# Optimization experiments

Measured on AMD Instinct MI355X. Metric: run time of the kernel, lower is better.

Reference implementation:

```python
import jax, jax.numpy as jnp
import numpy as np

# Mistral-7B layer-0 config
D, DKV, DFF, NH, NKV, HD, BLK, VOCAB = 4096, 1024, 14336, 32, 8, 128, 64, 32000
THETA = 10000.0
NF4_CODE = jnp.array([-1.0, -0.6961928009986877, -0.5250730514526367, -0.39491748809814453,
                      -0.28444138169288635, -0.18477343022823334, -0.09105003625154495, 0.0,
                      0.07958029955625534, 0.16093020141124725, 0.24611230194568634,
                      0.33791524171829224, 0.44070982933044434, 0.5626170039176941,
                      0.7229568362236023, 1.0], dtype=jnp.float32)


def dequant_nf4(idx, absmax):
    # idx: int [out,in] 4-bit codes; absmax: [numel/BLK] blockwise scales
    w = jnp.take(NF4_CODE, idx.reshape(-1, BLK)) * absmax[:, None]
    return w.reshape(idx.shape)


def rmsnorm(x, w, eps=1e-5):
    return x * jax.lax.rsqrt(jnp.mean(x * x, axis=-1, keepdims=True) + eps) * w


def rope(x, pos):
    # x: [B,S,H,HD] -- HF rotate-half convention
    half = HD // 2
    inv = 1.0 / (THETA ** (jnp.arange(0, half, dtype=jnp.float32) / half))
    f = pos[:, None] * inv[None, :]                      # [S, half]
    cos = jnp.concatenate([jnp.cos(f), jnp.cos(f)], -1)[None, :, None, :]
    sin = jnp.concatenate([jnp.sin(f), jnp.sin(f)], -1)[None, :, None, :]
    x1, x2 = x[..., :half], x[..., half:]
    rot = jnp.concatenate([-x2, x1], -1)
    return x * cos + rot * sin


def setup_inputs() -> dict:
    key = jax.random.key(0)
    ks = jax.random.split(key, 20)
    B, S = 4, 512
    inp = {}
    inp["input_ids"] = jax.random.randint(ks[0], (B, S), 0, VOCAB, dtype=jnp.int32)
    inp["attention_mask"] = jnp.ones((B, S), dtype=jnp.int32)
    inp["embed_table"] = jax.random.normal(ks[1], (VOCAB, D), dtype=jnp.float32) * 0.02
    shapes = {"q": (D, D), "k": (DKV, D), "v": (DKV, D), "o": (D, D),
              "gate": (DFF, D), "up": (DFF, D), "down": (D, DFF)}
    for i, (n, sh) in enumerate(shapes.items()):
        inp["idx_" + n] = jax.random.randint(ks[2 + i], sh, 0, 16, dtype=jnp.int32)
        inp["absmax_" + n] = jax.random.uniform(ks[9 + i], (sh[0] * sh[1] // BLK,), dtype=jnp.float32) * 0.02
    inp["rms1_w"] = jnp.ones((D,), jnp.float32)
    inp["rms2_w"] = jnp.ones((D,), jnp.float32)
    inp["dp_w"] = jax.random.normal(ks[16], (50, D), jnp.float32) * 0.02
    inp["dp_b"] = jnp.zeros((50,), jnp.float32)
    return inp


def reference(input_ids, attention_mask, embed_table,
              idx_q, idx_k, idx_v, idx_o, idx_gate, idx_up, idx_down,
              absmax_q, absmax_k, absmax_v, absmax_o, absmax_gate, absmax_up, absmax_down,
              rms1_w, rms2_w, dp_w, dp_b):
    B, S = input_ids.shape
    h = embed_table[input_ids]                            # [B,S,D]

    # --- Mistral decoder layer 0 (hidden_states[1]) ---
    r = rmsnorm(h, rms1_w)
    Wq = dequant_nf4(idx_q, absmax_q)
    Wk = dequant_nf4(idx_k, absmax_k)
    Wv = dequant_nf4(idx_v, absmax_v)
    Wo = dequant_nf4(idx_o, absmax_o)
    q = (r @ Wq.T).reshape(B, S, NH, HD)
    k = (r @ Wk.T).reshape(B, S, NKV, HD)
    v = (r @ Wv.T).reshape(B, S, NKV, HD)
    pos = jnp.arange(S, dtype=jnp.float32)
    q, k = rope(q, pos), rope(k, pos)
    rep = NH // NKV
    k = jnp.repeat(k, rep, axis=2)
    v = jnp.repeat(v, rep, axis=2)
    scores = jnp.einsum('bqhd,bkhd->bhqk', q, k) / np.float32(np.sqrt(HD))
    causal = jnp.tril(jnp.ones((S, S), bool))
    m = causal[None, None] & (attention_mask[:, None, None, :] > 0)
    scores = jnp.where(m, scores, jnp.float32(-1e9))
    p = jax.nn.softmax(scores, axis=-1)
    ao = jnp.einsum('bhqk,bkhd->bqhd', p, v).reshape(B, S, D)
    h = h + ao @ Wo.T

    r2 = rmsnorm(h, rms2_w)
    Wg = dequant_nf4(idx_gate, absmax_gate)
    Wu = dequant_nf4(idx_up, absmax_up)
    Wd = dequant_nf4(idx_down, absmax_down)
    h = h + (jax.nn.silu(r2 @ Wg.T) * (r2 @ Wu.T)) @ Wd.T

    # --- last_token_pool + L2 normalize ---
    last = jnp.sum(attention_mask, axis=-1) - 1           # [B]
    pooled = h[jnp.arange(B), last]                       # [B,D]
    pooled = pooled / jnp.maximum(jnp.linalg.norm(pooled, axis=1, keepdims=True), 1e-12)

    # --- down_projection + query*entity node embeddings ---
    emb = pooled @ dp_w.T + dp_b                          # [B,50]
    bs = B // 2
    node = emb[:bs] * emb[bs:]                            # [bs,50]
    return node
```

## Files before the change

kernel.cpp:

```cpp
#include <hip/hip_runtime.h>
#include <stdint.h>
#include <math.h>

#define TOK 2048
#define DMODEL 4096
#define DFF 14336
#define SEQ 512

typedef float f32x4 __attribute__((ext_vector_type(4)));
typedef short s16x8 __attribute__((ext_vector_type(8)));
typedef unsigned short u16x8 __attribute__((ext_vector_type(8)));

__constant__ float NF4_TAB[16] = {
  -1.0f, -0.6961928009986877f, -0.5250730514526367f, -0.39491748809814453f,
  -0.28444138169288635f, -0.18477343022823334f, -0.09105003625154495f, 0.0f,
  0.07958029955625534f, 0.16093020141124725f, 0.24611230194568634f,
  0.33791524171829224f, 0.44070982933044434f, 0.5626170039176941f,
  0.7229568362236023f, 1.0f };

__device__ __forceinline__ uint16_t f2bf(float f) {
  union { float f; uint32_t u; } x; x.f = f;
  uint32_t r = (x.u + 0x7FFFu + ((x.u >> 16) & 1u)) >> 16;
  return (uint16_t)r;
}
__device__ __forceinline__ float bf2f(uint16_t u) {
  union { uint32_t u; float f; } x; x.u = ((uint32_t)u) << 16;
  return x.f;
}
__device__ __forceinline__ f32x4 mfma16(s16x8 a, s16x8 b, f32x4 c) {
  return __builtin_amdgcn_mfma_f32_16x16x32_bf16(a, b, c, 0, 0, 0);
}
__device__ __forceinline__ void gload_lds16(const void* g, void* l) {
  __builtin_amdgcn_global_load_lds(
    (const __attribute__((address_space(1))) unsigned int*)g,
    (__attribute__((address_space(3))) unsigned int*)l, 16, 0, 0);
}

__global__ __launch_bounds__(256) void k_last(const int* __restrict__ maskp,
                                              int* __restrict__ lastb)
{
  int wv = threadIdx.x >> 6, l = threadIdx.x & 63;
  int cnt = 0;
  for (int j = l; j < SEQ; j += 64) cnt += (maskp[wv * SEQ + j] > 0);
  #pragma unroll
  for (int off = 1; off < 64; off <<= 1) cnt += __shfl_xor(cnt, off);
  if (l == 0) lastb[wv] = cnt - 1;
}

__global__ __launch_bounds__(256) void k_dequant(const int* __restrict__ idx,
    const float* __restrict__ am, uint16_t* __restrict__ out, int nelems, int K)
{
  __shared__ float code[16];
  if (threadIdx.x < 16) code[threadIdx.x] = NF4_TAB[threadIdx.x];
  __syncthreads();
  int nch = nelems >> 3;
  int stride = gridDim.x * 256;
  for (int c = blockIdx.x * 256 + threadIdx.x; c < nch; c += stride) {
    int e = c << 3;
    int row = e / K;
    int kc = e - row * K;
    float a = am[c >> 3];
    int4 i0 = *(const int4*)(idx + e);
    int4 i1 = *(const int4*)(idx + e + 4);
    u16x8 pk;
    pk[0] = f2bf(code[i0.x] * a);
    pk[1] = f2bf(code[i0.y] * a);
    pk[2] = f2bf(code[i0.z] * a);
    pk[3] = f2bf(code[i0.w] * a);
    pk[4] = f2bf(code[i1.x] * a);
    pk[5] = f2bf(code[i1.y] * a);
    pk[6] = f2bf(code[i1.z] * a);
    pk[7] = f2bf(code[i1.w] * a);
    int dk = (kc & ~63) | (((((kc >> 3) & 7) ^ (row & 7))) << 3);
    *(u16x8*)(out + (size_t)row * K + dk) = pk;
  }
}

__global__ __launch_bounds__(256) void k_rms(const int* __restrict__ ids,
    const float* __restrict__ table, const float* __restrict__ w,
    uint16_t* __restrict__ r)
{
  int t = blockIdx.x, tid = threadIdx.x;
  int wv = tid >> 6, l = tid & 63;
  const float* src = table + (size_t)ids[t] * DMODEL;
  int d0 = tid * 16;
  float vals[16];
  float ss = 0.f;
  #pragma unroll
  for (int i = 0; i < 4; ++i) {
    float4 v4 = *(const float4*)(src + d0 + i * 4);
    vals[i*4+0] = v4.x; vals[i*4+1] = v4.y; vals[i*4+2] = v4.z; vals[i*4+3] = v4.w;
    ss += v4.x*v4.x + v4.y*v4.y + v4.z*v4.z + v4.w*v4.w;
  }
  #pragma unroll
  for (int off = 1; off < 64; off <<= 1) ss += __shfl_xor(ss, off);
  __shared__ float red[4];
  if (l == 0) red[wv] = ss;
  __syncthreads();
  float rs = rsqrtf((red[0]+red[1]+red[2]+red[3]) * (1.f/DMODEL) + 1e-5f);
  #pragma unroll
  for (int cth = 0; cth < 2; ++cth) {
    int dd = d0 + cth * 8;
    u16x8 pk;
    #pragma unroll
    for (int j = 0; j < 8; ++j) pk[j] = f2bf(vals[cth*8+j] * rs * w[dd + j]);
    int dsw = (dd & ~63) | (((((dd >> 3) & 7) ^ (t & 7))) << 3);
    *(u16x8*)(r + (size_t)t * DMODEL + dsw) = pk;
  }
}

__global__ __launch_bounds__(512, 2) void k_gemmkv(
    const uint16_t* __restrict__ A, const uint16_t* __restrict__ W,
    float* __restrict__ pout)
{
  constexpr int K = 4096;
  constexpr int NT = 16;
  __shared__ __align__(1024) uint16_t As_[2 * 256 * 64];
  __shared__ __align__(1024) uint16_t Bs_[2 * 256 * 64];
  const int tid = threadIdx.x;
  const int wid = tid >> 6, l = tid & 63;
  const int wr = wid >> 2, wc = wid & 3;
  const int n0 = blockIdx.x * 256, m0 = blockIdx.y * 256;
  const size_t kbase = blockIdx.z * 1024;
  const int lrow = l >> 3, lcb = (l & 7) * 16;

  auto stA = [&](int t, int h) {
    int ta = (t < NT) ? t : (t - NT);
    const char* g = (const char*)A +
        ((size_t)(m0 + h * 128 + wid * 16 + lrow) * K + kbase + ta * 64) * 2 + lcb;
    char* s = (char*)As_ + (t & 1) * 32768 + h * 16384 + wid * 2048;
    gload_lds16(g, s);
    gload_lds16(g + (size_t)8 * K * 2, s + 1024);
  };
  auto stB = [&](int t, int h) {
    int ta = (t < NT) ? t : (t - NT);
    const char* g = (const char*)W +
        ((size_t)(n0 + h * 128 + wid * 16 + lrow) * K + kbase + ta * 64) * 2 + lcb;
    char* s = (char*)Bs_ + (t & 1) * 32768 + h * 16384 + wid * 2048;
    gload_lds16(g, s);
    gload_lds16(g + (size_t)8 * K * 2, s + 1024);
  };

  const int cb0 = (((l >> 4) << 4)) ^ ((l & 7) << 4);
  const int cb1 = (64 + ((l >> 4) << 4)) ^ ((l & 7) << 4);

  const f32x4 Z4 = {0.f, 0.f, 0.f, 0.f};
  f32x4 acc[8][4];
  #pragma unroll
  for (int i = 0; i < 8; ++i)
    #pragma unroll
    for (int j = 0; j < 4; ++j) acc[i][j] = Z4;
  s16x8 bfr[4][2];

#define VMW asm volatile("s_waitcnt vmcnt(6)" ::: "memory")
#define PHASE(DB, Q, READB, STG) {                                          \
    const char* abase = (const char*)As_ + (DB) * 32768;                    \
    s16x8 af[2][2];                                                         \
    _Pragma("unroll") for (int mm = 0; mm < 2; ++mm) {                      \
      int arow = ((2 * (2 * (Q) + mm) + wr) * 16 + (l & 15)) * 128;         \
      af[mm][0] = *(const s16x8*)(abase + arow + cb0);                      \
      af[mm][1] = *(const s16x8*)(abase + arow + cb1);                      \
    }                                                                       \
    if (READB) {                                                            \
      const char* bbase = (const char*)Bs_ + (DB) * 32768;                  \
      _Pragma("unroll") for (int nn = 0; nn < 4; ++nn) {                    \
        int brow = (wc * 64 + nn * 16 + (l & 15)) * 128;                    \
        bfr[nn][0] = *(const s16x8*)(bbase + brow + cb0);                   \
        bfr[nn][1] = *(const s16x8*)(bbase + brow + cb1);                   \
      }                                                                     \
    }                                                                       \
    STG;                                                                    \
    __builtin_amdgcn_s_barrier();                                           \
    asm volatile("s_waitcnt lgkmcnt(0)" ::: "memory");                      \
    __builtin_amdgcn_sched_barrier(0);                                      \
    __builtin_amdgcn_s_setprio(1);                                          \
    _Pragma("unroll") for (int mm = 0; mm < 2; ++mm)                        \
      _Pragma("unroll") for (int nn = 0; nn < 4; ++nn) {                    \
        acc[2 * (Q) + mm][nn] = mfma16(af[mm][0], bfr[nn][0], acc[2 * (Q) + mm][nn]); \
        acc[2 * (Q) + mm][nn] = mfma16(af[mm][1], bfr[nn][1], acc[2 * (Q) + mm][nn]); \
      }                                                                     \
    __builtin_amdgcn_s_setprio(0);                                          \
    __builtin_amdgcn_s_barrier();                                           \
  }

  stB(0, 0); stA(0, 0); stB(0, 1); stA(0, 1);
  stB(1, 0); stA(1, 0); stB(1, 1);
  VMW;
  __builtin_amdgcn_s_barrier();

  for (int it = 0; it < NT / 2; ++it) {
    int t0 = 2 * it, t1 = t0 + 1;
    PHASE(0, 0, 1, stA(t1, 1));
    PHASE(0, 1, 0, stB(t0 + 2, 0));
    PHASE(0, 2, 0, stA(t0 + 2, 0));
    PHASE(0, 3, 0, { stB(t0 + 2, 1); VMW; });
    PHASE(1, 0, 1, stA(t0 + 2, 1));
    PHASE(1, 1, 0, stB(t1 + 2, 0));
    PHASE(1, 2, 0, stA(t1 + 2, 0));
    PHASE(1, 3, 0, { stB(t1 + 2, 1); VMW; });
  }
  asm volatile("s_waitcnt vmcnt(0)" ::: "memory");
  __builtin_amdgcn_s_barrier();
#undef PHASE
#undef VMW

  float* po = pout + (size_t)blockIdx.z * 2048 * 2048;
  #pragma unroll
  for (int mf = 0; mf < 8; ++mf)
    #pragma unroll
    for (int nf = 0; nf < 4; ++nf)
      #pragma unroll
      for (int r = 0; r < 4; ++r) {
        int row = m0 + (2 * mf + wr) * 16 + ((l >> 4) << 2) + r;
        int col = n0 + wc * 64 + nf * 16 + (l & 15);
        po[(size_t)row * 2048 + col] = acc[mf][nf][r];
      }
}

__global__ __launch_bounds__(256) void k_redrope(const float* __restrict__ p,
    uint16_t* __restrict__ kv)
{
  int t = blockIdx.x, tid = threadIdx.x;
  const size_t zs = (size_t)2048 * 2048;
  auto sum4 = [&](int c) -> float {
    size_t o = (size_t)t * 2048 + c;
    return p[o] + p[o + zs] + p[o + 2 * zs] + p[o + 3 * zs];
  };
  float pos = (float)(t & (SEQ - 1));
  for (int pi = tid; pi < 512; pi += 256) {
    int hh = pi >> 6, j = pi & 63;
    int c1 = hh * 128 + j, c2 = c1 + 64;
    float s1 = sum4(c1), s2 = sum4(c2);
    float f = pos * expf(-(float)j * 0.14391156831212787f);
    float sn, cs;
    sincosf(f, &sn, &cs);
    kv[(size_t)t * 2048 + c1] = f2bf(s1 * cs - s2 * sn);
    kv[(size_t)t * 2048 + c2] = f2bf(s2 * cs + s1 * sn);
  }
  for (int c = 1024 + tid; c < 2048; c += 256)
    kv[(size_t)t * 2048 + c] = f2bf(sum4(c));
}

__global__ __launch_bounds__(256) void k_prep_r4(const uint16_t* __restrict__ rbuf,
    const int* __restrict__ lastb, float* __restrict__ r4i)
{
  int r = blockIdx.x;
  int t = r * SEQ + lastb[r];
  const uint16_t* src = rbuf + (size_t)t * DMODEL;
  for (int k = threadIdx.x * 8; k < DMODEL; k += 2048) {
    int so = (k & ~63) | (((((k >> 3) & 7) ^ (t & 7))) << 3);
    u16x8 v = *(const u16x8*)(src + so);
    #pragma unroll
    for (int j = 0; j < 8; ++j) r4i[(k + j) * 4 + r] = bf2f(v[j]);
  }
}

template<int MODE>
__global__ __launch_bounds__(256) void k_gemv4i(const int* __restrict__ idx,
    const float* __restrict__ am, const float* __restrict__ a4i,
    float* __restrict__ out4i, const float* __restrict__ table,
    const int* __restrict__ ids, const int* __restrict__ lastb)
{
  __shared__ float code[16];
  if (threadIdx.x < 16) code[threadIdx.x] = NF4_TAB[threadIdx.x];
  __syncthreads();
  int wv = threadIdx.x >> 6, l = threadIdx.x & 63;
  int lhi = l >> 4;
  int n = blockIdx.x * 4 + wv;
  const int4* ip = (const int4*)(idx + (size_t)n * 4096);
  const float* ap = am + (size_t)n * 64;
  float a0 = 0.f, a1 = 0.f, a2 = 0.f, a3 = 0.f;
  #pragma unroll
  for (int kk = 0; kk < 16; ++kk) {
    int4 iv = ip[kk * 64 + l];
    float sc = ap[kk * 4 + lhi];
    float w0 = code[iv.x] * sc, w1 = code[iv.y] * sc;
    float w2 = code[iv.z] * sc, w3 = code[iv.w] * sc;
    const float* A0 = a4i + (kk * 256 + l * 4) * 4;
    f32x4 k0 = *(const f32x4*)(A0);
    f32x4 k1 = *(const f32x4*)(A0 + 4);
    f32x4 k2 = *(const f32x4*)(A0 + 8);
    f32x4 k3 = *(const f32x4*)(A0 + 12);
    a0 = fmaf(w0, k0[0], fmaf(w1, k1[0], fmaf(w2, k2[0], fmaf(w3, k3[0], a0))));
    a1 = fmaf(w0, k0[1], fmaf(w1, k1[1], fmaf(w2, k2[1], fmaf(w3, k3[1], a1))));
    a2 = fmaf(w0, k0[2], fmaf(w1, k1[2], fmaf(w2, k2[2], fmaf(w3, k3[2], a2))));
    a3 = fmaf(w0, k0[3], fmaf(w1, k1[3], fmaf(w2, k2[3], fmaf(w3, k3[3], a3))));
  }
  #pragma unroll
  for (int off = 1; off < 64; off <<= 1) {
    a0 += __shfl_xor(a0, off); a1 += __shfl_xor(a1, off);
    a2 += __shfl_xor(a2, off); a3 += __shfl_xor(a3, off);
  }
  if (l == 0) {
    f32x4 o;
    o[0] = a0; o[1] = a1; o[2] = a2; o[3] = a3;
    if (MODE == 1) {
      #pragma unroll
      for (int r = 0; r < 4; ++r)
        o[r] += table[(size_t)ids[r * SEQ + lastb[r]] * DMODEL + n];
    }
    *(f32x4*)(out4i + (size_t)n * 4) = o;
  }
}

__global__ __launch_bounds__(256) void k_gemv_gu(const int* __restrict__ idxg,
    const float* __restrict__ amg, const int* __restrict__ idxu,
    const float* __restrict__ amu, const float* __restrict__ a4i,
    float* __restrict__ hm4i)
{
  __shared__ float code[16];
  if (threadIdx.x < 16) code[threadIdx.x] = NF4_TAB[threadIdx.x];
  __syncthreads();
  int wv = threadIdx.x >> 6, l = threadIdx.x & 63;
  int lhi = l >> 4;
  int n = blockIdx.x * 4 + wv;
  const int4* ipg = (const int4*)(idxg + (size_t)n * 4096);
  const int4* ipu = (const int4*)(idxu + (size_t)n * 4096);
  const float* apg = amg + (size_t)n * 64;
  const float* apu = amu + (size_t)n * 64;
  float g0 = 0.f, g1 = 0.f, g2 = 0.f, g3 = 0.f;
  float u0 = 0.f, u1 = 0.f, u2 = 0.f, u3 = 0.f;
  #pragma unroll
  for (int kk = 0; kk < 16; ++kk) {
    int4 ig = ipg[kk * 64 + l];
    int4 iu = ipu[kk * 64 + l];
    float sg = apg[kk * 4 + lhi];
    float su = apu[kk * 4 + lhi];
    float wg0 = code[ig.x] * sg, wg1 = code[ig.y] * sg;
    float wg2 = code[ig.z] * sg, wg3 = code[ig.w] * sg;
    float wu0 = code[iu.x] * su, wu1 = code[iu.y] * su;
    float wu2 = code[iu.z] * su, wu3 = code[iu.w] * su;
    const float* A0 = a4i + (kk * 256 + l * 4) * 4;
    f32x4 k0 = *(const f32x4*)(A0);
    f32x4 k1 = *(const f32x4*)(A0 + 4);
    f32x4 k2 = *(const f32x4*)(A0 + 8);
    f32x4 k3 = *(const f32x4*)(A0 + 12);
    g0 = fmaf(wg0, k0[0], fmaf(wg1, k1[0], fmaf(wg2, k2[0], fmaf(wg3, k3[0], g0))));
    g1 = fmaf(wg0, k0[1], fmaf(wg1, k1[1], fmaf(wg2, k2[1], fmaf(wg3, k3[1], g1))));
    g2 = fmaf(wg0, k0[2], fmaf(wg1, k1[2], fmaf(wg2, k2[2], fmaf(wg3, k3[2], g2))));
    g3 = fmaf(wg0, k0[3], fmaf(wg1, k1[3], fmaf(wg2, k2[3], fmaf(wg3, k3[3], g3))));
    u0 = fmaf(wu0, k0[0], fmaf(wu1, k1[0], fmaf(wu2, k2[0], fmaf(wu3, k3[0], u0))));
    u1 = fmaf(wu0, k0[1], fmaf(wu1, k1[1], fmaf(wu2, k2[1], fmaf(wu3, k3[1], u1))));
    u2 = fmaf(wu0, k0[2], fmaf(wu1, k1[2], fmaf(wu2, k2[2], fmaf(wu3, k3[2], u2))));
    u3 = fmaf(wu0, k0[3], fmaf(wu1, k1[3], fmaf(wu2, k2[3], fmaf(wu3, k3[3], u3))));
  }
  #pragma unroll
  for (int off = 1; off < 64; off <<= 1) {
    g0 += __shfl_xor(g0, off); g1 += __shfl_xor(g1, off);
    g2 += __shfl_xor(g2, off); g3 += __shfl_xor(g3, off);
    u0 += __shfl_xor(u0, off); u1 += __shfl_xor(u1, off);
    u2 += __shfl_xor(u2, off); u3 += __shfl_xor(u3, off);
  }
  if (l == 0) {
    f32x4 o;
    o[0] = (g0 / (1.f + __expf(-g0))) * u0;
    o[1] = (g1 / (1.f + __expf(-g1))) * u1;
    o[2] = (g2 / (1.f + __expf(-g2))) * u2;
    o[3] = (g3 / (1.f + __expf(-g3))) * u3;
    *(f32x4*)(hm4i + (size_t)n * 4) = o;
  }
}

__global__ __launch_bounds__(256) void k_gemv_down(const int* __restrict__ idx,
    const float* __restrict__ am, const float* __restrict__ hm4i,
    const float* __restrict__ h4i, float* __restrict__ h4r)
{
  __shared__ float code[16];
  if (threadIdx.x < 16) code[threadIdx.x] = NF4_TAB[threadIdx.x];
  __syncthreads();
  int wv = threadIdx.x >> 6, l = threadIdx.x & 63;
  int lhi = l >> 4;
  int n = blockIdx.x * 4 + wv;
  const int4* ip = (const int4*)(idx + (size_t)n * 14336);
  const float* ap = am + (size_t)n * 224;
  float a0 = 0.f, a1 = 0.f, a2 = 0.f, a3 = 0.f;
  #pragma unroll 8
  for (int kk = 0; kk < 56; ++kk) {
    int4 iv = ip[kk * 64 + l];
    float sc = ap[kk * 4 + lhi];
    float w0 = code[iv.x] * sc, w1 = code[iv.y] * sc;
    float w2 = code[iv.z] * sc, w3 = code[iv.w] * sc;
    const float* A0 = hm4i + (kk * 256 + l * 4) * 4;
    f32x4 k0 = *(const f32x4*)(A0);
    f32x4 k1 = *(const f32x4*)(A0 + 4);
    f32x4 k2 = *(const f32x4*)(A0 + 8);
    f32x4 k3 = *(const f32x4*)(A0 + 12);
    a0 = fmaf(w0, k0[0], fmaf(w1, k1[0], fmaf(w2, k2[0], fmaf(w3, k3[0], a0))));
    a1 = fmaf(w0, k0[1], fmaf(w1, k1[1], fmaf(w2, k2[1], fmaf(w3, k3[1], a1))));
    a2 = fmaf(w0, k0[2], fmaf(w1, k1[2], fmaf(w2, k2[2], fmaf(w3, k3[2], a2))));
    a3 = fmaf(w0, k0[3], fmaf(w1, k1[3], fmaf(w2, k2[3], fmaf(w3, k3[3], a3))));
  }
  #pragma unroll
  for (int off = 1; off < 64; off <<= 1) {
    a0 += __shfl_xor(a0, off); a1 += __shfl_xor(a1, off);
    a2 += __shfl_xor(a2, off); a3 += __shfl_xor(a3, off);
  }
  if (l == 0) {
    f32x4 hr = *(const f32x4*)(h4i + (size_t)n * 4);
    h4r[0 * 4096 + n] = hr[0] + a0;
    h4r[1 * 4096 + n] = hr[1] + a1;
    h4r[2 * 4096 + n] = hr[2] + a2;
    h4r[3 * 4096 + n] = hr[3] + a3;
  }
}

__global__ __launch_bounds__(256) void k_attn4(const float* __restrict__ q4i,
    const uint16_t* __restrict__ kv, const int* __restrict__ maskp,
    const int* __restrict__ lastb, float* __restrict__ ao4i)
{
  int hh = blockIdx.x, b = blockIdx.y;
  int kvh = hh >> 2;
  int tid = threadIdx.x;
  __shared__ float qs[128];
  __shared__ float sarr[512];
  __shared__ float red[256];
  __shared__ float oacc[2][128];
  int last = lastb[b];
  if (tid < 128) {
    int d = tid, j = d & 63;
    float f = (float)last * expf(-(float)j * 0.14391156831212787f);
    float sn, cs;
    sincosf(f, &sn, &cs);
    float qd  = q4i[(hh * 128 + d) * 4 + b];
    float qd2 = (d < 64) ? q4i[(hh * 128 + d + 64) * 4 + b]
                         : q4i[(hh * 128 + d - 64) * 4 + b];
    float v = (d < 64) ? (qd * cs - qd2 * sn) : (qd * cs + qd2 * sn);
    qs[d] = v * 0.08838834764831845f;
  }
  __syncthreads();
  float sl[2];
  #pragma unroll
  for (int h2 = 0; h2 < 2; ++h2) {
    int jj = tid + h2 * 256;
    bool valid = (jj <= last) && (maskp[b * SEQ + jj] > 0);
    float s = -1e9f;
    if (valid) {
      s = 0.f;
      const uint16_t* kp = kv + ((size_t)(b * SEQ + jj)) * 2048 + kvh * 128;
      #pragma unroll
      for (int c = 0; c < 16; ++c) {
        u16x8 kvv = *(const u16x8*)(kp + c * 8);
        #pragma unroll
        for (int e = 0; e < 8; ++e)
          s = fmaf(qs[c * 8 + e], bf2f(kvv[e]), s);
      }
    }
    sarr[jj] = s;
    sl[h2] = s;
  }
  red[tid] = fmaxf(sl[0], sl[1]);
  __syncthreads();
  for (int s = 128; s > 0; s >>= 1) {
    if (tid < s) red[tid] = fmaxf(red[tid], red[tid + s]);
    __syncthreads();
  }
  float m = red[0];
  __syncthreads();
  float ps = 0.f;
  #pragma unroll
  for (int h2 = 0; h2 < 2; ++h2) {
    int jj = tid + h2 * 256;
    float pe = __expf(sarr[jj] - m);
    ps += pe;
    sarr[jj] = pe;
  }
  red[tid] = ps;
  __syncthreads();
  for (int s = 128; s > 0; s >>= 1) {
    if (tid < s) red[tid] += red[tid + s];
    __syncthreads();
  }
  float inv = 1.f / red[0];
  __syncthreads();
  int half = tid >> 7, d = tid & 127;
  float acc = 0.f;
  const uint16_t* vp = kv + ((size_t)(b * SEQ + half * 256)) * 2048 + 1024 + kvh * 128 + d;
  for (int j = 0; j < 256; ++j)
    acc = fmaf(sarr[half * 256 + j], bf2f(vp[(size_t)j * 2048]), acc);
  oacc[half][d] = acc;
  __syncthreads();
  if (tid < 128)
    ao4i[(hh * 128 + tid) * 4 + b] = (oacc[0][tid] + oacc[1][tid]) * inv;
}

__global__ __launch_bounds__(256) void k_rms2i(const float* __restrict__ h4i,
    const float* __restrict__ w, float* __restrict__ r2i)
{
  int tid = threadIdx.x, wv = tid >> 6, l = tid & 63;
  f32x4 vals[16];
  f32x4 ss = {0.f, 0.f, 0.f, 0.f};
  #pragma unroll
  for (int i = 0; i < 16; ++i) {
    vals[i] = *(const f32x4*)(h4i + (size_t)(tid + i * 256) * 4);
    ss += vals[i] * vals[i];
  }
  #pragma unroll
  for (int off = 1; off < 64; off <<= 1) {
    ss[0] += __shfl_xor(ss[0], off);
    ss[1] += __shfl_xor(ss[1], off);
    ss[2] += __shfl_xor(ss[2], off);
    ss[3] += __shfl_xor(ss[3], off);
  }
  __shared__ f32x4 red[4];
  if (l == 0) red[wv] = ss;
  __syncthreads();
  f32x4 tot = red[0] + red[1] + red[2] + red[3];
  f32x4 rs;
  #pragma unroll
  for (int r = 0; r < 4; ++r) rs[r] = rsqrtf(tot[r] * (1.f / 4096.f) + 1e-5f);
  #pragma unroll
  for (int i = 0; i < 16; ++i) {
    float wk = w[tid + i * 256];
    f32x4 o = vals[i] * rs * wk;
    *(f32x4*)(r2i + (size_t)(tid + i * 256) * 4) = o;
  }
}

__global__ __launch_bounds__(256) void k_pool3(const float* __restrict__ h4r,
    const float* __restrict__ dpw, const float* __restrict__ dpb,
    float* __restrict__ out)
{
  int o = blockIdx.x;
  int tid = threadIdx.x, wv = tid >> 6, l = tid & 63;
  __shared__ float dsh[4], nsh[4];
  const float* row = h4r + wv * 4096;
  const float* wrow = dpw + (size_t)o * 4096;
  float d1 = 0.f, ss = 0.f;
  for (int d = l * 4; d < 4096; d += 256) {
    float4 v = *(const float4*)(row + d);
    float4 u = *(const float4*)(wrow + d);
    d1 += v.x*u.x + v.y*u.y + v.z*u.z + v.w*u.w;
    ss += v.x*v.x + v.y*v.y + v.z*v.z + v.w*v.w;
  }
  #pragma unroll
  for (int off = 1; off < 64; off <<= 1) {
    d1 += __shfl_xor(d1, off);
    ss += __shfl_xor(ss, off);
  }
  if (l == 0) { dsh[wv] = d1; nsh[wv] = fmaxf(sqrtf(ss), 1e-12f); }
  __syncthreads();
  if (tid < 2) {
    float b = dpb[o];
    float e1 = dsh[tid] / nsh[tid] + b;
    float e2 = dsh[tid + 2] / nsh[tid + 2] + b;
    out[tid * 50 + o] = e1 * e2;
  }
}

extern "C" void kernel_launch(void* const* d_in, const int* in_sizes, int n_in,
                              void* d_out, int out_size, void* d_ws, size_t ws_size,
                              hipStream_t stream) {
  const int*   ids   = (const int*)d_in[0];
  const int*   maskp = (const int*)d_in[1];
  const float* table = (const float*)d_in[2];
  const int* idxp[7];
  const float* amp[7];
  if (in_sizes[4] == in_sizes[3] / 64) {
    for (int i = 0; i < 7; ++i) {
      idxp[i] = (const int*)d_in[3 + 2 * i];
      amp[i]  = (const float*)d_in[4 + 2 * i];
    }
  } else {
    for (int i = 0; i < 7; ++i) {
      idxp[i] = (const int*)d_in[3 + i];
      amp[i]  = (const float*)d_in[10 + i];
    }
  }
  const float* rms1 = (const float*)d_in[17];
  const float* rms2w = (const float*)d_in[18];
  const float* dpw  = (const float*)d_in[19];
  const float* dpb  = (const float*)d_in[20];
  float* out = (float*)d_out;

  char* p = (char*)d_ws;
  int*      lastb = (int*)p;      p += 256;
  float*    r4i   = (float*)p;    p += 4 * 4096 * 4;
  float*    q4i   = (float*)p;    p += 4 * 4096 * 4;
  float*    ao4i  = (float*)p;    p += 4 * 4096 * 4;
  float*    h4i   = (float*)p;    p += 4 * 4096 * 4;
  float*    r2i   = (float*)p;    p += 4 * 4096 * 4;
  float*    h4r   = (float*)p;    p += 4 * 4096 * 4;
  float*    hm4i  = (float*)p;    p += (size_t)4 * DFF * 4 + 512;
  uint16_t* kvbuf = (uint16_t*)p; p += (size_t)TOK * 2048 * 2;
  uint16_t* rbuf  = (uint16_t*)p; p += (size_t)TOK * DMODEL * 2;
  uint16_t* wbuf  = (uint16_t*)p; p += (size_t)2048 * DMODEL * 2;
  float*    pbuf  = (float*)p;    p += (size_t)4 * 2048 * 2048 * 4;

  k_last<<<1, 256, 0, stream>>>(maskp, lastb);
  k_rms<<<TOK, 256, 0, stream>>>(ids, table, rms1, rbuf);

  k_dequant<<<2048, 256, 0, stream>>>(idxp[1], amp[1], wbuf, 1024 * DMODEL, DMODEL);
  k_dequant<<<2048, 256, 0, stream>>>(idxp[2], amp[2], wbuf + (size_t)1024 * DMODEL, 1024 * DMODEL, DMODEL);
  k_gemmkv<<<dim3(8, 8, 4), 512, 0, stream>>>(rbuf, wbuf, pbuf);
  k_redrope<<<TOK, 256, 0, stream>>>(pbuf, kvbuf);

  k_prep_r4<<<4, 256, 0, stream>>>(rbuf, lastb, r4i);
  k_gemv4i<0><<<1024, 256, 0, stream>>>(idxp[0], amp[0], r4i, q4i, nullptr, nullptr, nullptr);

  k_attn4<<<dim3(32, 4), 256, 0, stream>>>(q4i, kvbuf, maskp, lastb, ao4i);

  k_gemv4i<1><<<1024, 256, 0, stream>>>(idxp[3], amp[3], ao4i, h4i, table, ids, lastb);

  k_rms2i<<<1, 256, 0, stream>>>(h4i, rms2w, r2i);
  k_gemv_gu<<<3584, 256, 0, stream>>>(idxp[4], amp[4], idxp[5], amp[5], r2i, hm4i);
  k_gemv_down<<<1024, 256, 0, stream>>>(idxp[6], amp[6], hm4i, h4i, h4r);

  k_pool3<<<50, 256, 0, stream>>>(h4r, dpw, dpb, out);
}
```

Before: 415.6 us.

## Merge independent kernels into block-range fused launches and use packed f32x2 FMAs

```diff
diff --git a/kernel.cpp b/kernel.cpp
--- a/kernel.cpp
+++ b/kernel.cpp
@@ -8,6 +8,7 @@
 #define SEQ 512
 
 typedef float f32x4 __attribute__((ext_vector_type(4)));
+typedef float f32x2 __attribute__((ext_vector_type(2)));
 typedef short s16x8 __attribute__((ext_vector_type(8)));
 typedef unsigned short u16x8 __attribute__((ext_vector_type(8)));
 
@@ -35,77 +36,85 @@
     (const __attribute__((address_space(1))) unsigned int*)g,
     (__attribute__((address_space(3))) unsigned int*)l, 16, 0, 0);
 }
-
-__global__ __launch_bounds__(256) void k_last(const int* __restrict__ maskp,
-                                              int* __restrict__ lastb)
-{
-  int wv = threadIdx.x >> 6, l = threadIdx.x & 63;
-  int cnt = 0;
-  for (int j = l; j < SEQ; j += 64) cnt += (maskp[wv * SEQ + j] > 0);
-  #pragma unroll
-  for (int off = 1; off < 64; off <<= 1) cnt += __shfl_xor(cnt, off);
-  if (l == 0) lastb[wv] = cnt - 1;
-}
-
-__global__ __launch_bounds__(256) void k_dequant(const int* __restrict__ idx,
-    const float* __restrict__ am, uint16_t* __restrict__ out, int nelems, int K)
-{
-  __shared__ float code[16];
-  if (threadIdx.x < 16) code[threadIdx.x] = NF4_TAB[threadIdx.x];
-  __syncthreads();
-  int nch = nelems >> 3;
-  int stride = gridDim.x * 256;
-  for (int c = blockIdx.x * 256 + threadIdx.x; c < nch; c += stride) {
-    int e = c << 3;
-    int row = e / K;
-    int kc = e - row * K;
-    float a = am[c >> 3];
-    int4 i0 = *(const int4*)(idx + e);
-    int4 i1 = *(const int4*)(idx + e + 4);
-    u16x8 pk;
-    pk[0] = f2bf(code[i0.x] * a);
-    pk[1] = f2bf(code[i0.y] * a);
-    pk[2] = f2bf(code[i0.z] * a);
-    pk[3] = f2bf(code[i0.w] * a);
-    pk[4] = f2bf(code[i1.x] * a);
-    pk[5] = f2bf(code[i1.y] * a);
-    pk[6] = f2bf(code[i1.z] * a);
-    pk[7] = f2bf(code[i1.w] * a);
-    int dk = (kc & ~63) | (((((kc >> 3) & 7) ^ (row & 7))) << 3);
-    *(u16x8*)(out + (size_t)row * K + dk) = pk;
-  }
-}
-
-__global__ __launch_bounds__(256) void k_rms(const int* __restrict__ ids,
-    const float* __restrict__ table, const float* __restrict__ w,
-    uint16_t* __restrict__ r)
-{
-  int t = blockIdx.x, tid = threadIdx.x;
-  int wv = tid >> 6, l = tid & 63;
-  const float* src = table + (size_t)ids[t] * DMODEL;
-  int d0 = tid * 16;
-  float vals[16];
-  float ss = 0.f;
-  #pragma unroll
-  for (int i = 0; i < 4; ++i) {
-    float4 v4 = *(const float4*)(src + d0 + i * 4);
-    vals[i*4+0] = v4.x; vals[i*4+1] = v4.y; vals[i*4+2] = v4.z; vals[i*4+3] = v4.w;
-    ss += v4.x*v4.x + v4.y*v4.y + v4.z*v4.z + v4.w*v4.w;
-  }
-  #pragma unroll
-  for (int off = 1; off < 64; off <<= 1) ss += __shfl_xor(ss, off);
-  __shared__ float red[4];
-  if (l == 0) red[wv] = ss;
-  __syncthreads();
-  float rs = rsqrtf((red[0]+red[1]+red[2]+red[3]) * (1.f/DMODEL) + 1e-5f);
-  #pragma unroll
-  for (int cth = 0; cth < 2; ++cth) {
-    int dd = d0 + cth * 8;
-    u16x8 pk;
-    #pragma unroll
-    for (int j = 0; j < 8; ++j) pk[j] = f2bf(vals[cth*8+j] * rs * w[dd + j]);
-    int dsw = (dd & ~63) | (((((dd >> 3) & 7) ^ (t & 7))) << 3);
-    *(u16x8*)(r + (size_t)t * DMODEL + dsw) = pk;
+__device__ __forceinline__ f32x2 pf(float w, f32x2 v, f32x2 acc) {
+  f32x2 wv = {w, w};
+  return wv * v + acc;
+}
+
+__global__ __launch_bounds__(256) void k_fusedA(const int* __restrict__ ids,
+    const float* __restrict__ table, const float* __restrict__ w1,
+    uint16_t* __restrict__ rbuf, const int* __restrict__ idxK,
+    const float* __restrict__ amK, const int* __restrict__ idxV,
+    const float* __restrict__ amV, uint16_t* __restrict__ wbuf,
+    const int* __restrict__ maskp, int* __restrict__ lastb)
+{
+  int bid = blockIdx.x, tid = threadIdx.x;
+  if (bid < 2048) {
+    int t = bid;
+    int wv = tid >> 6, l = tid & 63;
+    const float* src = table + (size_t)ids[t] * DMODEL;
+    int d0 = tid * 16;
+    float vals[16];
+    float ss = 0.f;
+    #pragma unroll
+    for (int i = 0; i < 4; ++i) {
+      float4 v4 = *(const float4*)(src + d0 + i * 4);
+      vals[i*4+0] = v4.x; vals[i*4+1] = v4.y; vals[i*4+2] = v4.z; vals[i*4+3] = v4.w;
+      ss += v4.x*v4.x + v4.y*v4.y + v4.z*v4.z + v4.w*v4.w;
+    }
+    #pragma unroll
+    for (int off = 1; off < 64; off <<= 1) ss += __shfl_xor(ss, off);
+    __shared__ float red[4];
+    if (l == 0) red[wv] = ss;
+    __syncthreads();
+    float rs = rsqrtf((red[0]+red[1]+red[2]+red[3]) * (1.f/DMODEL) + 1e-5f);
+    #pragma unroll
+    for (int cth = 0; cth < 2; ++cth) {
+      int dd = d0 + cth * 8;
+      u16x8 pk;
+      #pragma unroll
+      for (int j = 0; j < 8; ++j) pk[j] = f2bf(vals[cth*8+j] * rs * w1[dd + j]);
+      int dsw = (dd & ~63) | (((((dd >> 3) & 7) ^ (t & 7))) << 3);
+      *(u16x8*)(rbuf + (size_t)t * DMODEL + dsw) = pk;
+    }
+  } else if (bid < 3072) {
+    bool isV = bid >= 2560;
+    const int* idx = isV ? idxV : idxK;
+    const float* am = isV ? amV : amK;
+    uint16_t* out = wbuf + (isV ? (size_t)1024 * DMODEL : 0);
+    int base = bid - (isV ? 2560 : 2048);
+    __shared__ float code[16];
+    if (tid < 16) code[tid] = NF4_TAB[tid];
+    __syncthreads();
+    const int nch = 1024 * DMODEL / 8;
+    for (int c = base * 256 + tid; c < nch; c += 512 * 256) {
+      int e = c << 3;
+      int row = e >> 12;
+      int kc = e & 4095;
+      float a = am[c >> 3];
+      int4 i0 = *(const int4*)(idx + e);
+      int4 i1 = *(const int4*)(idx + e + 4);
+      u16x8 pk;
+      pk[0] = f2bf(code[i0.x] * a);
+      pk[1] = f2bf(code[i0.y] * a);
+      pk[2] = f2bf(code[i0.z] * a);
+      pk[3] = f2bf(code[i0.w] * a);
+      pk[4] = f2bf(code[i1.x] * a);
+      pk[5] = f2bf(code[i1.y] * a);
+      pk[6] = f2bf(code[i1.z] * a);
+      pk[7] = f2bf(code[i1.w] * a);
+      int dk = (kc & ~63) | (((((kc >> 3) & 7) ^ (row & 7))) << 3);
+      *(u16x8*)(out + (size_t)row * DMODEL + dk) = pk;
+    }
+  } else {
+    int b = bid - 3072;
+    if (tid < 64) {
+      int cnt = 0;
+      for (int j = tid; j < SEQ; j += 64) cnt += (maskp[b * SEQ + j] > 0);
+      #pragma unroll
+      for (int off = 1; off < 64; off <<= 1) cnt += __shfl_xor(cnt, off);
+      if (tid == 0) lastb[b] = cnt - 1;
+    }
   }
 }
 
@@ -120,8 +129,12 @@
   const int tid = threadIdx.x;
   const int wid = tid >> 6, l = tid & 63;
   const int wr = wid >> 2, wc = wid & 3;
-  const int n0 = blockIdx.x * 256, m0 = blockIdx.y * 256;
-  const size_t kbase = blockIdx.z * 1024;
+  int f = blockIdx.x + (blockIdx.y << 3) + (blockIdx.z << 6);
+  int fs = ((f & 7) << 5) + (f >> 3);
+  const int n0 = (fs & 7) * 256;
+  const int m0 = ((fs >> 3) & 7) * 256;
+  const int zq = fs >> 6;
+  const size_t kbase = (size_t)zq * 1024;
   const int lrow = l >> 3, lcb = (l & 7) * 16;
 
   auto stA = [&](int t, int h) {
@@ -204,7 +217,7 @@
 #undef PHASE
 #undef VMW
 
-  float* po = pout + (size_t)blockIdx.z * 2048 * 2048;
+  float* po = pout + (size_t)zq * 2048 * 2048;
   #pragma unroll
   for (int mf = 0; mf < 8; ++mf)
     #pragma unroll
@@ -217,30 +230,6 @@
       }
 }
 
-__global__ __launch_bounds__(256) void k_redrope(const float* __restrict__ p,
-    uint16_t* __restrict__ kv)
-{
-  int t = blockIdx.x, tid = threadIdx.x;
-  const size_t zs = (size_t)2048 * 2048;
-  auto sum4 = [&](int c) -> float {
-    size_t o = (size_t)t * 2048 + c;
-    return p[o] + p[o + zs] + p[o + 2 * zs] + p[o + 3 * zs];
-  };
-  float pos = (float)(t & (SEQ - 1));
-  for (int pi = tid; pi < 512; pi += 256) {
-    int hh = pi >> 6, j = pi & 63;
-    int c1 = hh * 128 + j, c2 = c1 + 64;
-    float s1 = sum4(c1), s2 = sum4(c2);
-    float f = pos * expf(-(float)j * 0.14391156831212787f);
-    float sn, cs;
-    sincosf(f, &sn, &cs);
-    kv[(size_t)t * 2048 + c1] = f2bf(s1 * cs - s2 * sn);
-    kv[(size_t)t * 2048 + c2] = f2bf(s2 * cs + s1 * sn);
-  }
-  for (int c = 1024 + tid; c < 2048; c += 256)
-    kv[(size_t)t * 2048 + c] = f2bf(sum4(c));
-}
-
 __global__ __launch_bounds__(256) void k_prep_r4(const uint16_t* __restrict__ rbuf,
     const int* __restrict__ lastb, float* __restrict__ r4i)
 {
@@ -255,8 +244,77 @@
   }
 }
 
-template<int MODE>
-__global__ __launch_bounds__(256) void k_gemv4i(const int* __restrict__ idx,
+__global__ __launch_bounds__(256) void k_fusedD(const float* __restrict__ p,
+    uint16_t* __restrict__ kv, const int* __restrict__ idxQ,
+    const float* __restrict__ amQ, const float* __restrict__ a4i,
+    float* __restrict__ q4i)
+{
+  int bid = blockIdx.x, tid = threadIdx.x;
+  if (bid < 2048) {
+    int t = bid;
+    const size_t zs = (size_t)2048 * 2048;
+    auto sum4 = [&](int c) -> float {
+      size_t o = (size_t)t * 2048 + c;
+      return p[o] + p[o + zs] + p[o + 2 * zs] + p[o + 3 * zs];
+    };
+    float pos = (float)(t & (SEQ - 1));
+    for (int pi = tid; pi < 512; pi += 256) {
+      int hh = pi >> 6, j = pi & 63;
+      int c1 = hh * 128 + j, c2 = c1 + 64;
+      float s1 = sum4(c1), s2 = sum4(c2);
+      float f = pos * expf(-(float)j * 0.14391156831212787f);
+      float sn, cs;
+      sincosf(f, &sn, &cs);
+      kv[(size_t)t * 2048 + c1] = f2bf(s1 * cs - s2 * sn);
+      kv[(size_t)t * 2048 + c2] = f2bf(s2 * cs + s1 * sn);
+    }
+    for (int c = 1024 + tid; c < 2048; c += 256)
+      kv[(size_t)t * 2048 + c] = f2bf(sum4(c));
+  } else {
+    __shared__ float code[16];
+    if (tid < 16) code[tid] = NF4_TAB[tid];
+    __syncthreads();
+    int wv = tid >> 6, l = tid & 63;
+    int lhi = l >> 4;
+    int n = (bid - 2048) * 4 + wv;
+    const int4* ip = (const int4*)(idxQ + (size_t)n * 4096);
+    const float* ap = amQ + (size_t)n * 64;
+    f32x2 a01 = {0.f, 0.f}, a23 = {0.f, 0.f};
+    #pragma unroll
+    for (int kk = 0; kk < 16; ++kk) {
+      int4 iv = ip[kk * 64 + l];
+      float sc = ap[kk * 4 + lhi];
+      float w0 = code[iv.x] * sc, w1 = code[iv.y] * sc;
+      float w2 = code[iv.z] * sc, w3 = code[iv.w] * sc;
+      const float* A0 = a4i + (kk * 256 + l * 4) * 4;
+      f32x4 k0 = *(const f32x4*)(A0);
+      f32x4 k1 = *(const f32x4*)(A0 + 4);
+      f32x4 k2 = *(const f32x4*)(A0 + 8);
+      f32x4 k3 = *(const f32x4*)(A0 + 12);
+      a01 = pf(w0, __builtin_shufflevector(k0, k0, 0, 1), a01);
+      a23 = pf(w0, __builtin_shufflevector(k0, k0, 2, 3), a23);
+      a01 = pf(w1, __builtin_shufflevector(k1, k1, 0, 1), a01);
+      a23 = pf(w1, __builtin_shufflevector(k1, k1, 2, 3), a23);
+      a01 = pf(w2, __builtin_shufflevector(k2, k2, 0, 1), a01);
+      a23 = pf(w2, __builtin_shufflevector(k2, k2, 2, 3), a23);
+      a01 = pf(w3, __builtin_shufflevector(k3, k3, 0, 1), a01);
+      a23 = pf(w3, __builtin_shufflevector(k3, k3, 2, 3), a23);
+    }
+    float a0 = a01[0], a1 = a01[1], a2 = a23[0], a3 = a23[1];
+    #pragma unroll
+    for (int off = 1; off < 64; off <<= 1) {
+      a0 += __shfl_xor(a0, off); a1 += __shfl_xor(a1, off);
+      a2 += __shfl_xor(a2, off); a3 += __shfl_xor(a3, off);
+    }
+    if (l == 0) {
+      f32x4 o;
+      o[0] = a0; o[1] = a1; o[2] = a2; o[3] = a3;
+      *(f32x4*)(q4i + (size_t)n * 4) = o;
+    }
+  }
+}
+
+__global__ __launch_bounds__(256) void k_gemv_o(const int* __restrict__ idx,
     const float* __restrict__ am, const float* __restrict__ a4i,
     float* __restrict__ out4i, const float* __restrict__ table,
     const int* __restrict__ ids, const int* __restrict__ lastb)
@@ -269,7 +327,7 @@
   int n = blockIdx.x * 4 + wv;
   const int4* ip = (const int4*)(idx + (size_t)n * 4096);
   const float* ap = am + (size_t)n * 64;
-  float a0 = 0.f, a1 = 0.f, a2 = 0.f, a3 = 0.f;
+  f32x2 a01 = {0.f, 0.f}, a23 = {0.f, 0.f};
   #pragma unroll
   for (int kk = 0; kk < 16; ++kk) {
     int4 iv = ip[kk * 64 + l];
@@ -281,11 +339,16 @@
     f32x4 k1 = *(const f32x4*)(A0 + 4);
     f32x4 k2 = *(const f32x4*)(A0 + 8);
     f32x4 k3 = *(const f32x4*)(A0 + 12);
-    a0 = fmaf(w0, k0[0], fmaf(w1, k1[0], fmaf(w2, k2[0], fmaf(w3, k3[0], a0))));
-    a1 = fmaf(w0, k0[1], fmaf(w1, k1[1], fmaf(w2, k2[1], fmaf(w3, k3[1], a1))));
-    a2 = fmaf(w0, k0[2], fmaf(w1, k1[2], fmaf(w2, k2[2], fmaf(w3, k3[2], a2))));
-    a3 = fmaf(w0, k0[3], fmaf(w1, k1[3], fmaf(w2, k2[3], fmaf(w3, k3[3], a3))));
-  }
+    a01 = pf(w0, __builtin_shufflevector(k0, k0, 0, 1), a01);
+    a23 = pf(w0, __builtin_shufflevector(k0, k0, 2, 3), a23);
+    a01 = pf(w1, __builtin_shufflevector(k1, k1, 0, 1), a01);
+    a23 = pf(w1, __builtin_shufflevector(k1, k1, 2, 3), a23);
+    a01 = pf(w2, __builtin_shufflevector(k2, k2, 0, 1), a01);
+    a23 = pf(w2, __builtin_shufflevector(k2, k2, 2, 3), a23);
+    a01 = pf(w3, __builtin_shufflevector(k3, k3, 0, 1), a01);
+    a23 = pf(w3, __builtin_shufflevector(k3, k3, 2, 3), a23);
+  }
+  float a0 = a01[0], a1 = a01[1], a2 = a23[0], a3 = a23[1];
   #pragma unroll
   for (int off = 1; off < 64; off <<= 1) {
     a0 += __shfl_xor(a0, off); a1 += __shfl_xor(a1, off);
@@ -294,11 +357,9 @@
   if (l == 0) {
     f32x4 o;
     o[0] = a0; o[1] = a1; o[2] = a2; o[3] = a3;
-    if (MODE == 1) {
-      #pragma unroll
-      for (int r = 0; r < 4; ++r)
-        o[r] += table[(size_t)ids[r * SEQ + lastb[r]] * DMODEL + n];
-    }
+    #pragma unroll
+    for (int r = 0; r < 4; ++r)
+      o[r] += table[(size_t)ids[r * SEQ + lastb[r]] * DMODEL + n];
     *(f32x4*)(out4i + (size_t)n * 4) = o;
   }
 }
@@ -318,9 +379,9 @@
   const int4* ipu = (const int4*)(idxu + (size_t)n * 4096);
   const float* apg = amg + (size_t)n * 64;
   const float* apu = amu + (size_t)n * 64;
-  float g0 = 0.f, g1 = 0.f, g2 = 0.f, g3 = 0.f;
-  float u0 = 0.f, u1 = 0.f, u2 = 0.f, u3 = 0.f;
-  #pragma unroll
+  f32x2 g01 = {0.f, 0.f}, g23 = {0.f, 0.f};
+  f32x2 u01 = {0.f, 0.f}, u23 = {0.f, 0.f};
+  #pragma unroll 8
   for (int kk = 0; kk < 16; ++kk) {
     int4 ig = ipg[kk * 64 + l];
     int4 iu = ipu[kk * 64 + l];
@@ -335,15 +396,21 @@
     f32x4 k1 = *(const f32x4*)(A0 + 4);
     f32x4 k2 = *(const f32x4*)(A0 + 8);
     f32x4 k3 = *(const f32x4*)(A0 + 12);
-    g0 = fmaf(wg0, k0[0], fmaf(wg1, k1[0], fmaf(wg2, k2[0], fmaf(wg3, k3[0], g0))));
-    g1 = fmaf(wg0, k0[1], fmaf(wg1, k1[1], fmaf(wg2, k2[1], fmaf(wg3, k3[1], g1))));
-    g2 = fmaf(wg0, k0[2], fmaf(wg1, k1[2], fmaf(wg2, k2[2], fmaf(wg3, k3[2], g2))));
-    g3 = fmaf(wg0, k0[3], fmaf(wg1, k1[3], fmaf(wg2, k2[3], fmaf(wg3, k3[3], g3))));
-    u0 = fmaf(wu0, k0[0], fmaf(wu1, k1[0], fmaf(wu2, k2[0], fmaf(wu3, k3[0], u0))));
-    u1 = fmaf(wu0, k0[1], fmaf(wu1, k1[1], fmaf(wu2, k2[1], fmaf(wu3, k3[1], u1))));
-    u2 = fmaf(wu0, k0[2], fmaf(wu1, k1[2], fmaf(wu2, k2[2], fmaf(wu3, k3[2], u2))));
-    u3 = fmaf(wu0, k0[3], fmaf(wu1, k1[3], fmaf(wu2, k2[3], fmaf(wu3, k3[3], u3))));
-  }
+    f32x2 k0l = __builtin_shufflevector(k0, k0, 0, 1), k0h = __builtin_shufflevector(k0, k0, 2, 3);
+    f32x2 k1l = __builtin_shufflevector(k1, k1, 0, 1), k1h = __builtin_shufflevector(k1, k1, 2, 3);
+    f32x2 k2l = __builtin_shufflevector(k2, k2, 0, 1), k2h = __builtin_shufflevector(k2, k2, 2, 3);
+    f32x2 k3l = __builtin_shufflevector(k3, k3, 0, 1), k3h = __builtin_shufflevector(k3, k3, 2, 3);
+    g01 = pf(wg0, k0l, g01); g23 = pf(wg0, k0h, g23);
+    g01 = pf(wg1, k1l, g01); g23 = pf(wg1, k1h, g23);
+    g01 = pf(wg2, k2l, g01); g23 = pf(wg2, k2h, g23);
+    g01 = pf(wg3, k3l, g01); g23 = pf(wg3, k3h, g23);
+    u01 = pf(wu0, k0l, u01); u23 = pf(wu0, k0h, u23);
+    u01 = pf(wu1, k1l, u01); u23 = pf(wu1, k1h, u23);
+    u01 = pf(wu2, k2l, u01); u23 = pf(wu2, k2h, u23);
+    u01 = pf(wu3, k3l, u01); u23 = pf(wu3, k3h, u23);
+  }
+  float g0 = g01[0], g1 = g01[1], g2 = g23[0], g3 = g23[1];
+  float u0 = u01[0], u1 = u01[1], u2 = u23[0], u3 = u23[1];
   #pragma unroll
   for (int off = 1; off < 64; off <<= 1) {
     g0 += __shfl_xor(g0, off); g1 += __shfl_xor(g1, off);
@@ -373,7 +440,7 @@
   int n = blockIdx.x * 4 + wv;
   const int4* ip = (const int4*)(idx + (size_t)n * 14336);
   const float* ap = am + (size_t)n * 224;
-  float a0 = 0.f, a1 = 0.f, a2 = 0.f, a3 = 0.f;
+  f32x2 a01 = {0.f, 0.f}, a23 = {0.f, 0.f};
   #pragma unroll 8
   for (int kk = 0; kk < 56; ++kk) {
     int4 iv = ip[kk * 64 + l];
@@ -385,11 +452,16 @@
     f32x4 k1 = *(const f32x4*)(A0 + 4);
     f32x4 k2 = *(const f32x4*)(A0 + 8);
     f32x4 k3 = *(const f32x4*)(A0 + 12);
-    a0 = fmaf(w0, k0[0], fmaf(w1, k1[0], fmaf(w2, k2[0], fmaf(w3, k3[0], a0))));
-    a1 = fmaf(w0, k0[1], fmaf(w1, k1[1], fmaf(w2, k2[1], fmaf(w3, k3[1], a1))));
-    a2 = fmaf(w0, k0[2], fmaf(w1, k1[2], fmaf(w2, k2[2], fmaf(w3, k3[2], a2))));
-    a3 = fmaf(w0, k0[3], fmaf(w1, k1[3], fmaf(w2, k2[3], fmaf(w3, k3[3], a3))));
-  }
+    a01 = pf(w0, __builtin_shufflevector(k0, k0, 0, 1), a01);
+    a23 = pf(w0, __builtin_shufflevector(k0, k0, 2, 3), a23);
+    a01 = pf(w1, __builtin_shufflevector(k1, k1, 0, 1), a01);
+    a23 = pf(w1, __builtin_shufflevector(k1, k1, 2, 3), a23);
+    a01 = pf(w2, __builtin_shufflevector(k2, k2, 0, 1), a01);
+    a23 = pf(w2, __builtin_shufflevector(k2, k2, 2, 3), a23);
+    a01 = pf(w3, __builtin_shufflevector(k3, k3, 0, 1), a01);
+    a23 = pf(w3, __builtin_shufflevector(k3, k3, 2, 3), a23);
+  }
+  float a0 = a01[0], a1 = a01[1], a2 = a23[0], a3 = a23[1];
   #pragma unroll
   for (int off = 1; off < 64; off <<= 1) {
     a0 += __shfl_xor(a0, off); a1 += __shfl_xor(a1, off);
@@ -414,7 +486,7 @@
   __shared__ float qs[128];
   __shared__ float sarr[512];
   __shared__ float red[256];
-  __shared__ float oacc[2][128];
+  __shared__ f32x2 oacc2[4][64];
   int last = lastb[b];
   if (tid < 128) {
     int d = tid, j = d & 63;
@@ -472,15 +544,24 @@
   }
   float inv = 1.f / red[0];
   __syncthreads();
-  int half = tid >> 7, d = tid & 127;
-  float acc = 0.f;
-  const uint16_t* vp = kv + ((size_t)(b * SEQ + half * 256)) * 2048 + 1024 + kvh * 128 + d;
-  for (int j = 0; j < 256; ++j)
-    acc = fmaf(sarr[half * 256 + j], bf2f(vp[(size_t)j * 2048]), acc);
-  oacc[half][d] = acc;
-  __syncthreads();
-  if (tid < 128)
-    ao4i[(hh * 128 + tid) * 4 + b] = (oacc[0][tid] + oacc[1][tid]) * inv;
+  int qd = tid >> 6, pr = tid & 63;
+  f32x2 acc = {0.f, 0.f};
+  const uint16_t* vp = kv + ((size_t)(b * SEQ + qd * 128)) * 2048 + 1024 + kvh * 128 + pr * 2;
+  for (int j = 0; j < 128; ++j) {
+    float pj = sarr[qd * 128 + j];
+    uint32_t pair = *(const uint32_t*)(vp + (size_t)j * 2048);
+    f32x2 v;
+    v[0] = bf2f((uint16_t)(pair & 0xffff));
+    v[1] = bf2f((uint16_t)(pair >> 16));
+    acc = pf(pj, v, acc);
+  }
+  oacc2[qd][pr] = acc;
+  __syncthreads();
+  if (tid < 64) {
+    f32x2 s = oacc2[0][tid] + oacc2[1][tid] + oacc2[2][tid] + oacc2[3][tid];
+    ao4i[((size_t)(hh * 128 + tid * 2)) * 4 + b]     = s[0] * inv;
+    ao4i[((size_t)(hh * 128 + tid * 2 + 1)) * 4 + b] = s[1] * inv;
+  }
 }
 
 __global__ __launch_bounds__(256) void k_rms2i(const float* __restrict__ h4i,
@@ -586,20 +667,18 @@
   uint16_t* wbuf  = (uint16_t*)p; p += (size_t)2048 * DMODEL * 2;
   float*    pbuf  = (float*)p;    p += (size_t)4 * 2048 * 2048 * 4;
 
-  k_last<<<1, 256, 0, stream>>>(maskp, lastb);
-  k_rms<<<TOK, 256, 0, stream>>>(ids, table, rms1, rbuf);
-
-  k_dequant<<<2048, 256, 0, stream>>>(idxp[1], amp[1], wbuf, 1024 * DMODEL, DMODEL);
-  k_dequant<<<2048, 256, 0, stream>>>(idxp[2], amp[2], wbuf + (size_t)1024 * DMODEL, 1024 * DMODEL, DMODEL);
+  k_fusedA<<<3076, 256, 0, stream>>>(ids, table, rms1, rbuf,
+      idxp[1], amp[1], idxp[2], amp[2], wbuf, maskp, lastb);
+
   k_gemmkv<<<dim3(8, 8, 4), 512, 0, stream>>>(rbuf, wbuf, pbuf);
-  k_redrope<<<TOK, 256, 0, stream>>>(pbuf, kvbuf);
 
   k_prep_r4<<<4, 256, 0, stream>>>(rbuf, lastb, r4i);
-  k_gemv4i<0><<<1024, 256, 0, stream>>>(idxp[0], amp[0], r4i, q4i, nullptr, nullptr, nullptr);
+
+  k_fusedD<<<3072, 256, 0, stream>>>(pbuf, kvbuf, idxp[0], amp[0], r4i, q4i);
 
   k_attn4<<<dim3(32, 4), 256, 0, stream>>>(q4i, kvbuf, maskp, lastb, ao4i);
 
-  k_gemv4i<1><<<1024, 256, 0, stream>>>(idxp[3], amp[3], ao4i, h4i, table, ids, lastb);
+  k_gemv_o<<<1024, 256, 0, stream>>>(idxp[3], amp[3], ao4i, h4i, table, ids, lastb);
 
   k_rms2i<<<1, 256, 0, stream>>>(h4i, rms2w, r2i);
   k_gemv_gu<<<3584, 256, 0, stream>>>(idxp[4], amp[4], idxp[5], amp[5], r2i, hm4i);
```

After: 390.3 us. 1.06x faster.
